# Kernel optimization log

Hardware: AMD Instinct MI355X
Metric: run time of the kernel (lower is better)

## Reference

```python
import jax, jax.numpy as jnp
import numpy as np

CVOCAB = 600  # static extended-vocab size (torch code uses max(src_map)+1; src_map values < 600)


def setup_inputs() -> dict:
    key = jax.random.key(0)
    k1, k2, k3, k4, k5 = jax.random.split(key, 5)
    N, D, V = 2048, 1024, 50257  # N = batch*tlen
    B, S = 32, 400               # batch, source length
    return {
        "hidden": jax.random.normal(k1, (N, D), jnp.float32),
        "orig_prob": jax.random.normal(k2, (N, V), jnp.float32),
        "attn": jax.random.uniform(k3, (N, S), jnp.float32),
        "src_map": jax.random.randint(k4, (B, S), 0, CVOCAB, jnp.int32),
        "W_copy": jax.random.normal(k5, (1, D), jnp.float32) * 0.02,
        "b_copy": jnp.zeros((1,), jnp.float32),
    }


def reference(hidden, orig_prob, attn, src_map, W_copy, b_copy):
    batch, slen = src_map.shape
    # p_softmax over target vocab
    prob = jax.nn.softmax(orig_prob, axis=1)                  # (N, V)
    # copy switch p(z=1)
    p_copy = jax.nn.sigmoid(hidden @ W_copy.T + b_copy)       # (N, 1)
    out_prob = prob * (1.0 - p_copy)                          # (N, V)
    mul_attn = (attn * p_copy).reshape(batch, -1, slen)       # (B, T, S)

    # one-hot + bmm in the original == scatter-add of attention mass into extended vocab slots
    def scatter_batch(a, sm):
        # a: (T, S), sm: (S,) -> (T, CVOCAB), duplicates accumulate
        return jnp.zeros((a.shape[0], CVOCAB), a.dtype).at[:, sm].add(a)

    copy_prob = jax.vmap(scatter_batch)(mul_attn, src_map)    # (B, T, CVOCAB)
    return out_prob, copy_prob.reshape(-1, CVOCAB)
```

## Files before the change

### kernel.cpp

```cpp
#include <hip/hip_runtime.h>
#include <math.h>

#define WAVE 64
#define BDIM 1024
#define NIT  13

typedef float f32x4 __attribute__((ext_vector_type(4)));

__global__ __launch_bounds__(BDIM, 4) void fused_kernel(
        const float* __restrict__ x,
        const float* __restrict__ hidden,
        const float* __restrict__ W,
        const float* __restrict__ bptr,
        const float* __restrict__ attn,
        const int*   __restrict__ src_map,
        float* __restrict__ out_prob,
        float* __restrict__ copy_out,
        int V, int D, int S, int C, int T) {
    const int row  = blockIdx.x;
    const int tid  = threadIdx.x;
    const int lane = tid & (WAVE - 1);
    const int wid  = tid / WAVE;

    __shared__ float red_sum[BDIM / WAVE];
    __shared__ float red_dot[BDIM / WAVE];
    extern __shared__ float bins[];

    for (int j = tid; j < C; j += BDIM) bins[j] = 0.f;

    const float* xr = x + (size_t)row * V;
    float v[NIT * 4];
    #pragma unroll
    for (int i = 0; i < NIT; ++i) {
        int e = (i * BDIM + tid) * 4;
        if (e + 3 < V) {
            float4 t = *(const float4*)(xr + e);
            v[4*i+0] = t.x; v[4*i+1] = t.y; v[4*i+2] = t.z; v[4*i+3] = t.w;
        } else {
            #pragma unroll
            for (int k = 0; k < 4; ++k)
                v[4*i+k] = (e + k < V) ? xr[e + k] : -INFINITY;
        }
    }

    float my_attn = 0.f; int my_slot = 0;
    if (tid < S) {
        my_attn = attn[(size_t)row * S + tid];
        my_slot = src_map[(size_t)(row / T) * S + tid];
    }

    float lsum = 0.f;
    #pragma unroll
    for (int j = 0; j < NIT * 4; ++j) {
        v[j] = __expf(v[j]);
        lsum += v[j];
    }

    float ldot = 0.f;
    {
        const float* h = hidden + (size_t)row * D;
        for (int e = tid; e < D; e += BDIM)
            ldot += h[e] * W[e];
    }

    #pragma unroll
    for (int off = 32; off >= 1; off >>= 1) {
        lsum += __shfl_xor(lsum, off, WAVE);
        ldot += __shfl_xor(ldot, off, WAVE);
    }
    if (lane == 0) { red_sum[wid] = lsum; red_dot[wid] = ldot; }
    __syncthreads();
    float s = 0.f, dd = 0.f;
    #pragma unroll
    for (int w = 0; w < BDIM / WAVE; ++w) { s += red_sum[w]; dd += red_dot[w]; }
    const float pc    = 1.f / (1.f + __expf(-(dd + bptr[0])));
    const float scale = (1.f - pc) / s;

    if (tid < S) atomicAdd(&bins[my_slot], my_attn * pc);
    __syncthreads();
    {
        float* outc = copy_out + (size_t)row * C;
        for (int j = tid; j < C; j += BDIM)
            outc[j] = bins[j];
    }

    float* outr = out_prob + (size_t)row * V;
    #pragma unroll
    for (int i = 0; i < NIT; ++i) {
        int e = (i * BDIM + tid) * 4;
        if (e + 3 < V) {
            f32x4 o;
            o.x = v[4*i+0] * scale; o.y = v[4*i+1] * scale;
            o.z = v[4*i+2] * scale; o.w = v[4*i+3] * scale;
            __builtin_nontemporal_store(o, (f32x4*)(outr + e));
        } else {
            #pragma unroll
            for (int k = 0; k < 4; ++k)
                if (e + k < V) outr[e + k] = v[4*i+k] * scale;
        }
    }
}

extern "C" void kernel_launch(void* const* d_in, const int* in_sizes, int n_in,
                              void* d_out, int out_size, void* d_ws, size_t ws_size,
                              hipStream_t stream) {
    const float* hidden  = (const float*)d_in[0];
    const float* orig    = (const float*)d_in[1];
    const float* attn    = (const float*)d_in[2];
    const int*   src_map = (const int*)  d_in[3];
    const float* W       = (const float*)d_in[4];
    const float* b       = (const float*)d_in[5];

    const int D = in_sizes[4];
    const int N = in_sizes[0] / D;
    const int V = in_sizes[1] / N;
    const int S = in_sizes[2] / N;
    const int B = in_sizes[3] / S;
    const int T = N / B;
    const int C = out_size / N - V;

    float* out_prob = (float*)d_out;
    float* copy_out = (float*)d_out + (size_t)N * V;

    fused_kernel<<<N, BDIM, C * sizeof(float), stream>>>(
        orig, hidden, W, b, attn, src_map, out_prob, copy_out, V, D, S, C, T);
}
```

Measured before the change: 185.4 us.

## Split each softmax row across two cooperating blocks with global-atomic reduction

Each row is now handled by two 512-thread blocks, each covering half the vocabulary. They combine their partial exp-sums and partial dot products through global atomics and spin on a per-row counter before scaling and writing. The aim is smaller blocks with more scheduling flexibility and lower register pressure per block. The cost is an extra memset launch, global atomics and a cross-block spin-wait, which relies on both blocks of a row being co-resident and can deadlock or stall if they are not.

```diff
diff --git a/kernel.cpp b/kernel.cpp
--- a/kernel.cpp
+++ b/kernel.cpp
@@ -2,8 +2,9 @@
 #include <math.h>
 
 #define WAVE 64
-#define BDIM 1024
-#define NIT  13
+#define BDIM 512
+#define NITH 13
+#define HSPLIT 25088
 
 typedef float f32x4 __attribute__((ext_vector_type(4)));
 
@@ -16,42 +17,52 @@
         const int*   __restrict__ src_map,
         float* __restrict__ out_prob,
         float* __restrict__ copy_out,
-        int V, int D, int S, int C, int T) {
-    const int row  = blockIdx.x;
+        float* __restrict__ wsum,
+        float* __restrict__ wdot,
+        int*   __restrict__ wcnt,
+        int N, int V, int D, int S, int C, int T) {
+    const int bid  = blockIdx.x;
+    const int row  = bid >> 1;
+    const int half = bid & 1;
     const int tid  = threadIdx.x;
     const int lane = tid & (WAVE - 1);
     const int wid  = tid / WAVE;
 
     __shared__ float red_sum[BDIM / WAVE];
     __shared__ float red_dot[BDIM / WAVE];
+    __shared__ float bcast[2];
     extern __shared__ float bins[];
 
-    for (int j = tid; j < C; j += BDIM) bins[j] = 0.f;
+    if (half == 0)
+        for (int j = tid; j < C; j += BDIM) bins[j] = 0.f;
+
+    const int base  = half ? HSPLIT : 0;
+    const int limit = half ? V : HSPLIT;
 
     const float* xr = x + (size_t)row * V;
-    float v[NIT * 4];
+    float v[NITH * 4];
     #pragma unroll
-    for (int i = 0; i < NIT; ++i) {
-        int e = (i * BDIM + tid) * 4;
-        if (e + 3 < V) {
+    for (int i = 0; i < NITH; ++i) {
+        int e = base + (i * BDIM + tid) * 4;
+        if (e + 3 < limit) {
             float4 t = *(const float4*)(xr + e);
             v[4*i+0] = t.x; v[4*i+1] = t.y; v[4*i+2] = t.z; v[4*i+3] = t.w;
         } else {
             #pragma unroll
             for (int k = 0; k < 4; ++k)
-                v[4*i+k] = (e + k < V) ? xr[e + k] : -INFINITY;
+                v[4*i+k] = (e + k < limit) ? xr[e + k] : -INFINITY;
         }
     }
 
     float my_attn = 0.f; int my_slot = 0;
-    if (tid < S) {
+    if (half == 0 && tid < S) {
         my_attn = attn[(size_t)row * S + tid];
         my_slot = src_map[(size_t)(row / T) * S + tid];
     }
 
     float lsum = 0.f;
     #pragma unroll
-    for (int j = 0; j < NIT * 4; ++j) {
+    for (int j = 0; j < NITH * 4; ++j) {
         v[j] = __expf(v[j]);
         lsum += v[j];
     }
@@ -59,7 +70,8 @@
     float ldot = 0.f;
     {
         const float* h = hidden + (size_t)row * D;
-        for (int e = tid; e < D; e += BDIM)
+        const int dh = D >> 1;
+        for (int e = half * dh + tid; e < (half + 1) * dh; e += BDIM)
             ldot += h[e] * W[e];
     }
 
@@ -70,15 +82,31 @@
     }
     if (lane == 0) { red_sum[wid] = lsum; red_dot[wid] = ldot; }
     __syncthreads();
-    float s = 0.f, dd = 0.f;
-    #pragma unroll
-    for (int w = 0; w < BDIM / WAVE; ++w) { s += red_sum[w]; dd += red_dot[w]; }
-    const float pc    = 1.f / (1.f + __expf(-(dd + bptr[0])));
-    const float scale = (1.f - pc) / s;
+    if (tid == 0) {
+        float s = 0.f, dd = 0.f;
+        #pragma unroll
+        for (int w = 0; w < BDIM / WAVE; ++w) { s += red_sum[w]; dd += red_dot[w]; }
+        atomicAdd(&wsum[row], s);
+        atomicAdd(&wdot[row], dd);
+        __threadfence();
+        atomicAdd(&wcnt[row], 1);
+        while (__hip_atomic_load(&wcnt[row], __ATOMIC_ACQUIRE,
+                                 __HIP_MEMORY_SCOPE_AGENT) < 2) { }
+        float st = __hip_atomic_load(&wsum[row], __ATOMIC_RELAXED,
+                                     __HIP_MEMORY_SCOPE_AGENT);
+        float dt = __hip_atomic_load(&wdot[row], __ATOMIC_RELAXED,
+                                     __HIP_MEMORY_SCOPE_AGENT);
+        float pc = 1.f / (1.f + __expf(-(dt + bptr[0])));
+        bcast[0] = (1.f - pc) / st;
+        bcast[1] = pc;
+    }
+    __syncthreads();
+    const float scale = bcast[0];
+    const float pc    = bcast[1];
 
-    if (tid < S) atomicAdd(&bins[my_slot], my_attn * pc);
-    __syncthreads();
-    {
+    if (half == 0) {
+        if (tid < S) atomicAdd(&bins[my_slot], my_attn * pc);
+        __syncthreads();
         float* outc = copy_out + (size_t)row * C;
         for (int j = tid; j < C; j += BDIM)
             outc[j] = bins[j];
@@ -86,9 +114,9 @@
 
     float* outr = out_prob + (size_t)row * V;
     #pragma unroll
-    for (int i = 0; i < NIT; ++i) {
-        int e = (i * BDIM + tid) * 4;
-        if (e + 3 < V) {
+    for (int i = 0; i < NITH; ++i) {
+        int e = base + (i * BDIM + tid) * 4;
+        if (e + 3 < limit) {
             f32x4 o;
             o.x = v[4*i+0] * scale; o.y = v[4*i+1] * scale;
             o.z = v[4*i+2] * scale; o.w = v[4*i+3] * scale;
@@ -96,7 +124,7 @@
         } else {
             #pragma unroll
             for (int k = 0; k < 4; ++k)
-                if (e + k < V) outr[e + k] = v[4*i+k] * scale;
+                if (e + k < limit) outr[e + k] = v[4*i+k] * scale;
         }
     }
 }
@@ -122,6 +150,12 @@
     float* out_prob = (float*)d_out;
     float* copy_out = (float*)d_out + (size_t)N * V;
 
-    fused_kernel<<<N, BDIM, C * sizeof(float), stream>>>(
-        orig, hidden, W, b, attn, src_map, out_prob, copy_out, V, D, S, C, T);
+    float* wsum = (float*)d_ws;
+    float* wdot = wsum + N;
+    int*   wcnt = (int*)(wdot + N);
+    hipMemsetAsync(d_ws, 0, (size_t)N * 12, stream);
+
+    fused_kernel<<<2 * N, BDIM, C * sizeof(float), stream>>>(
+        orig, hidden, W, b, attn, src_map, out_prob, copy_out,
+        wsum, wdot, wcnt, N, V, D, S, C, T);
 }
```

New measurement: 372.1 us. 101% more time.

## Replace register-cached softmax row with two-pass streaming recompute

Applied to the files above, without the earlier changes.

Instead of holding each row of logits in registers (52 floats per thread) across the reduction, the kernel now streams the row twice. The first pass accumulates the exp sum; the second reloads the logits, recomputes exp and writes scaled outputs. Block size drops to 512 and the occupancy hint rises to 8, with sched_barrier-grouped batches of 8 float4 loads to keep memory requests in flight. This lowers register pressure and raises occupancy, at the cost of reading the input row twice, which may only partly be served from cache.

```diff
diff --git a/kernel.cpp b/kernel.cpp
--- a/kernel.cpp
+++ b/kernel.cpp
@@ -2,12 +2,12 @@
 #include <math.h>
 
 #define WAVE 64
-#define BDIM 1024
-#define NIT  13
+#define BDIM 512
+#define GDEPTH 8
 
 typedef float f32x4 __attribute__((ext_vector_type(4)));
 
-__global__ __launch_bounds__(BDIM, 4) void fused_kernel(
+__global__ __launch_bounds__(BDIM, 8) void fused_kernel(
         const float* __restrict__ x,
         const float* __restrict__ hidden,
         const float* __restrict__ W,
@@ -29,19 +29,8 @@
     for (int j = tid; j < C; j += BDIM) bins[j] = 0.f;
 
     const float* xr = x + (size_t)row * V;
-    float v[NIT * 4];
-    #pragma unroll
-    for (int i = 0; i < NIT; ++i) {
-        int e = (i * BDIM + tid) * 4;
-        if (e + 3 < V) {
-            float4 t = *(const float4*)(xr + e);
-            v[4*i+0] = t.x; v[4*i+1] = t.y; v[4*i+2] = t.z; v[4*i+3] = t.w;
-        } else {
-            #pragma unroll
-            for (int k = 0; k < 4; ++k)
-                v[4*i+k] = (e + k < V) ? xr[e + k] : -INFINITY;
-        }
-    }
+    const int nv4   = V >> 2;
+    const int nfull = nv4 / BDIM;
 
     float my_attn = 0.f; int my_slot = 0;
     if (tid < S) {
@@ -50,10 +39,25 @@
     }
 
     float lsum = 0.f;
-    #pragma unroll
-    for (int j = 0; j < NIT * 4; ++j) {
-        v[j] = __expf(v[j]);
-        lsum += v[j];
+    for (int i = 0; i + GDEPTH <= nfull; i += GDEPTH) {
+        float4 t[GDEPTH];
+        #pragma unroll
+        for (int j = 0; j < GDEPTH; ++j)
+            t[j] = *(const float4*)(xr + (size_t)4 * ((i + j) * BDIM + tid));
+        __builtin_amdgcn_sched_barrier(0);
+        #pragma unroll
+        for (int j = 0; j < GDEPTH; ++j)
+            lsum += (__expf(t[j].x) + __expf(t[j].y)) +
+                    (__expf(t[j].z) + __expf(t[j].w));
+    }
+    {
+        const int e4 = nfull * BDIM + tid;
+        if (e4 < nv4) {
+            const float4 t = *(const float4*)(xr + (size_t)4 * e4);
+            lsum += (__expf(t.x) + __expf(t.y)) + (__expf(t.z) + __expf(t.w));
+        }
+        if (tid == 0)
+            for (int e = nv4 * 4; e < V; ++e) lsum += __expf(xr[e]);
     }
 
     float ldot = 0.f;
@@ -85,19 +89,33 @@
     }
 
     float* outr = out_prob + (size_t)row * V;
-    #pragma unroll
-    for (int i = 0; i < NIT; ++i) {
-        int e = (i * BDIM + tid) * 4;
-        if (e + 3 < V) {
+    for (int i = 0; i + GDEPTH <= nfull; i += GDEPTH) {
+        float4 t[GDEPTH];
+        #pragma unroll
+        for (int j = 0; j < GDEPTH; ++j)
+            t[j] = *(const float4*)(xr + (size_t)4 * ((i + j) * BDIM + tid));
+        __builtin_amdgcn_sched_barrier(0);
+        #pragma unroll
+        for (int j = 0; j < GDEPTH; ++j) {
             f32x4 o;
-            o.x = v[4*i+0] * scale; o.y = v[4*i+1] * scale;
-            o.z = v[4*i+2] * scale; o.w = v[4*i+3] * scale;
-            __builtin_nontemporal_store(o, (f32x4*)(outr + e));
-        } else {
-            #pragma unroll
-            for (int k = 0; k < 4; ++k)
-                if (e + k < V) outr[e + k] = v[4*i+k] * scale;
+            o.x = __expf(t[j].x) * scale; o.y = __expf(t[j].y) * scale;
+            o.z = __expf(t[j].z) * scale; o.w = __expf(t[j].w) * scale;
+            __builtin_nontemporal_store(o,
+                (f32x4*)(outr + (size_t)4 * ((i + j) * BDIM + tid)));
         }
+    }
+    {
+        const int e4 = nfull * BDIM + tid;
+        if (e4 < nv4) {
+            const float4 t = *(const float4*)(xr + (size_t)4 * e4);
+            f32x4 o;
+            o.x = __expf(t.x) * scale; o.y = __expf(t.y) * scale;
+            o.z = __expf(t.z) * scale; o.w = __expf(t.w) * scale;
+            __builtin_nontemporal_store(o, (f32x4*)(outr + (size_t)4 * e4));
+        }
+        if (tid == 0)
+            for (int e = nv4 * 4; e < V; ++e)
+                outr[e] = __expf(xr[e]) * scale;
     }
 }
 
```

After: 198.9 us. +7.3%, slower.
